# Kernel optimization log

Measured on AMD Instinct MI355X. Metric: run time of the kernel, lower is better.

The kernel has to match this reference:

```python
import jax, jax.numpy as jnp
import numpy as np

K = 5        # kernel_size
G = 1        # group_size
S = 2        # scale_factor
PAD = K // 2


def setup_inputs() -> dict:
    key = jax.random.key(0)
    k1, k2 = jax.random.split(key)
    N, C, H, W = 2, 256, 128, 128
    sH, sW = H * S, W * S
    features = jax.random.normal(k1, (N, C, H, W), dtype=jnp.float32)
    raw = jax.random.uniform(k2, (N, G * K * K, sH, sW), dtype=jnp.float32)
    # CARAFEPack softmax-normalizes masks over the k*k window per group; emulate that here
    m = raw.reshape(N, G, K * K, sH, sW)
    m = m / jnp.sum(m, axis=2, keepdims=True)
    masks = m.reshape(N, G * K * K, sH, sW)
    return {"features": features, "masks": masks}


def _carafe(features, masks):
    N, C, H, W = features.shape
    sH, sW = H * S, W * S
    Cg = C // G
    # zero-pad spatial dims so every output location has a full k x k neighborhood
    fpad = jnp.pad(features, ((0, 0), (0, 0), (PAD, PAD), (PAD, PAD)))  # [N,C,H+2p,W+2p]
    m = masks.reshape(N, G, K * K, sH, sW)
    out = jnp.zeros((N, G, Cg, sH, sW), dtype=features.dtype)
    # loop over the fixed k*k kernel offsets (25 iters): shift, nearest-upsample, weight, accumulate
    for di in range(K):
        for dj in range(K):
            shifted = fpad[:, :, di:di + H, dj:dj + W]                      # [N,C,H,W]
            up = jnp.repeat(jnp.repeat(shifted, S, axis=2), S, axis=3)      # [N,C,sH,sW] nearest upsample
            w = m[:, :, di * K + dj][:, :, None]                            # [N,G,1,sH,sW]
            out = out + up.reshape(N, G, Cg, sH, sW) * w
    return out.reshape(N, C, sH, sW)


def reference(features, masks):
    return _carafe(features, masks)
```

## Files before the change

### kernel.cpp

```cpp
#include <hip/hip_runtime.h>


namespace {
constexpr int N_ = 2, C_ = 256, H_ = 128, W_ = 128;
constexpr int K_ = 5, S_ = 2, PAD_ = 2;
constexpr int SH_ = H_ * S_, SW_ = W_ * S_;
constexpr int CPB = 16;
constexpr int TPB = 256;
constexpr int RPB = 2;
constexpr int HB_ = H_ / RPB;
constexpr int LW  = W_ + 2 * PAD_;
constexpr int LROWS = RPB + 2 * PAD_;
constexpr int LSZ = LROWS * LW;
constexpr int NSLOT = (LSZ + TPB - 1) / TPB;
typedef float v2f __attribute__((ext_vector_type(2)));
}

__device__ __forceinline__ void block_sync_lds() {
    __builtin_amdgcn_sched_barrier(0);
    asm volatile("s_waitcnt lgkmcnt(0)" ::: "memory");
    __builtin_amdgcn_s_barrier();
    __builtin_amdgcn_sched_barrier(0);
}

__global__ __launch_bounds__(TPB, 2) void carafe_kernel(
    const float* __restrict__ feat,
    const float* __restrict__ masks,
    float* __restrict__ out)
{
    __shared__ float lds[2][LSZ];

    const int bx = blockIdx.x;
    const int n  = bx / HB_;
    const int h0 = (bx % HB_) * RPB;
    const int t  = threadIdx.x;
    const int hl = t >> 7;
    const int w  = t & (W_ - 1);
    const int h  = h0 + hl;
    const int c0 = blockIdx.y * CPB;

    int  goff[NSLOT];
    bool gval[NSLOT];
#pragma unroll
    for (int s = 0; s < NSLOT; ++s) {
        int idx = s * TPB + t;
        int r  = idx / LW, cc = idx % LW;
        int gy = h0 - PAD_ + r, gx = cc - PAD_;
        bool ok = (idx < LSZ) && ((unsigned)gy < (unsigned)H_) && ((unsigned)gx < (unsigned)W_);
        gval[s] = ok;
        goff[s] = ok ? (gy * W_ + gx) : 0;
    }

    float m0[25], m1[25], m2[25], m3[25];
    {
        const float* mb = masks + ((size_t)n * 25) * (SH_ * SW_)
                                + (size_t)(S_ * h) * SW_ + S_ * w;
#pragma unroll
        for (int k = 0; k < 25; ++k) {
            v2f tt = *(const v2f*)(mb + (size_t)k * (SH_ * SW_));
            v2f bb = *(const v2f*)(mb + (size_t)k * (SH_ * SW_) + SW_);
            m0[k] = tt.x; m1[k] = tt.y; m2[k] = bb.x; m3[k] = bb.y;
        }
    }

    const float* fb = feat + ((size_t)n * C_ + c0) * (H_ * W_);
    float*       ob = out + (((size_t)n * C_ + c0) * SH_ + (size_t)(S_ * h)) * SW_ + S_ * w;

    auto issue = [&](int c, float* st) {
        const float* f = fb + (size_t)c * (H_ * W_);
#pragma unroll
        for (int s = 0; s < NSLOT; ++s) st[s] = gval[s] ? f[goff[s]] : 0.f;
    };
    auto land = [&](int b, const float* st) {
#pragma unroll
        for (int s = 0; s < NSLOT; ++s) {
            int idx = s * TPB + t;
            if (idx < LSZ) lds[b][idx] = st[s];
        }
    };
    auto compute_store = [&](const float* __restrict__ L, int c) {
        float a0 = 0.f, a1 = 0.f, a2 = 0.f, a3 = 0.f;
#pragma unroll
        for (int di = 0; di < K_; ++di) {
            const float* Lr = L + (hl + di) * LW + w;
            float f0 = Lr[0], f1 = Lr[1], f2 = Lr[2], f3 = Lr[3], f4 = Lr[4];
            const int kb = di * K_;
            a0 = fmaf(f0, m0[kb + 0], a0);
            a1 = fmaf(f0, m1[kb + 0], a1);
            a2 = fmaf(f0, m2[kb + 0], a2);
            a3 = fmaf(f0, m3[kb + 0], a3);
            a0 = fmaf(f1, m0[kb + 1], a0);
            a1 = fmaf(f1, m1[kb + 1], a1);
            a2 = fmaf(f1, m2[kb + 1], a2);
            a3 = fmaf(f1, m3[kb + 1], a3);
            a0 = fmaf(f2, m0[kb + 2], a0);
            a1 = fmaf(f2, m1[kb + 2], a1);
            a2 = fmaf(f2, m2[kb + 2], a2);
            a3 = fmaf(f2, m3[kb + 2], a3);
            a0 = fmaf(f3, m0[kb + 3], a0);
            a1 = fmaf(f3, m1[kb + 3], a1);
            a2 = fmaf(f3, m2[kb + 3], a2);
            a3 = fmaf(f3, m3[kb + 3], a3);
            a0 = fmaf(f4, m0[kb + 4], a0);
            a1 = fmaf(f4, m1[kb + 4], a1);
            a2 = fmaf(f4, m2[kb + 4], a2);
            a3 = fmaf(f4, m3[kb + 4], a3);
        }
        float* oc = ob + (size_t)c * ((size_t)SH_ * SW_);
        v2f top = {a0, a1}, bot = {a2, a3};
        __builtin_nontemporal_store(top, (v2f*)oc);
        __builtin_nontemporal_store(bot, (v2f*)(oc + SW_));
    };

    float stA[NSLOT], stB[NSLOT];
#pragma unroll
    for (int s = 0; s < NSLOT; ++s) {
        int idx = s * TPB + t;
        if (idx < LSZ) lds[0][idx] = gval[s] ? fb[goff[s]] : 0.f;
    }
    issue(1, stA);

    for (int c2 = 0; c2 < CPB; c2 += 2) {
        block_sync_lds();
        if (c2 + 2 < CPB) issue(c2 + 2, stB);
        compute_store(&lds[0][0], c2);
        land(1, stA);

        block_sync_lds();
        if (c2 + 3 < CPB) issue(c2 + 3, stA);
        compute_store(&lds[1][0], c2 + 1);
        if (c2 + 2 < CPB) land(0, stB);
    }
}

extern "C" void kernel_launch(void* const* d_in, const int* in_sizes, int n_in,
                              void* d_out, int out_size, void* d_ws, size_t ws_size,
                              hipStream_t stream) {
    const float* feat  = (const float*)d_in[0];
    const float* masks = (const float*)d_in[1];
    float* out = (float*)d_out;
    dim3 grid(N_ * HB_, C_ / CPB);
    carafe_kernel<<<grid, dim3(TPB), 0, stream>>>(feat, masks, out);
}
```

Baseline: 56.92 us.

## Double channels per pipeline stage and per block, switch to regular stores

Each pipeline stage now loads and computes two channels per LDS buffer instead of one, which halves the barrier count per channel. The block also covers twice as many channels, so mask registers are amortized over more work and the grid is smaller. Nontemporal output stores are replaced with plain vector stores. In exchange, LDS use and staging registers double and there are fewer blocks to fill the GPU.

```diff
diff --git a/kernel.cpp b/kernel.cpp
--- a/kernel.cpp
+++ b/kernel.cpp
@@ -5,7 +5,7 @@
 constexpr int N_ = 2, C_ = 256, H_ = 128, W_ = 128;
 constexpr int K_ = 5, S_ = 2, PAD_ = 2;
 constexpr int SH_ = H_ * S_, SW_ = W_ * S_;
-constexpr int CPB = 16;
+constexpr int CPB = 32;
 constexpr int TPB = 256;
 constexpr int RPB = 2;
 constexpr int HB_ = H_ / RPB;
@@ -28,7 +28,7 @@
     const float* __restrict__ masks,
     float* __restrict__ out)
 {
-    __shared__ float lds[2][LSZ];
+    __shared__ float lds[2][2 * LSZ];
 
     const int bx = blockIdx.x;
     const int n  = bx / HB_;
@@ -66,16 +66,24 @@
     const float* fb = feat + ((size_t)n * C_ + c0) * (H_ * W_);
     float*       ob = out + (((size_t)n * C_ + c0) * SH_ + (size_t)(S_ * h)) * SW_ + S_ * w;
 
-    auto issue = [&](int c, float* st) {
-        const float* f = fb + (size_t)c * (H_ * W_);
+    auto issue2 = [&](int c, float* st) {
+        const float* f0 = fb + (size_t)c * (H_ * W_);
+        const float* f1 = f0 + (H_ * W_);
 #pragma unroll
-        for (int s = 0; s < NSLOT; ++s) st[s] = gval[s] ? f[goff[s]] : 0.f;
+        for (int s = 0; s < NSLOT; ++s) st[s] = gval[s] ? f0[goff[s]] : 0.f;
+#pragma unroll
+        for (int s = 0; s < NSLOT; ++s) st[NSLOT + s] = gval[s] ? f1[goff[s]] : 0.f;
     };
-    auto land = [&](int b, const float* st) {
+    auto land2 = [&](int b, const float* st) {
 #pragma unroll
         for (int s = 0; s < NSLOT; ++s) {
             int idx = s * TPB + t;
             if (idx < LSZ) lds[b][idx] = st[s];
+        }
+#pragma unroll
+        for (int s = 0; s < NSLOT; ++s) {
+            int idx = s * TPB + t;
+            if (idx < LSZ) lds[b][LSZ + idx] = st[NSLOT + s];
         }
     };
     auto compute_store = [&](const float* __restrict__ L, int c) {
@@ -107,29 +115,33 @@
             a3 = fmaf(f4, m3[kb + 4], a3);
         }
         float* oc = ob + (size_t)c * ((size_t)SH_ * SW_);
-        v2f top = {a0, a1}, bot = {a2, a3};
-        __builtin_nontemporal_store(top, (v2f*)oc);
-        __builtin_nontemporal_store(bot, (v2f*)(oc + SW_));
+        *(v2f*)oc         = v2f{a0, a1};
+        *(v2f*)(oc + SW_) = v2f{a2, a3};
     };
 
-    float stA[NSLOT], stB[NSLOT];
+    float stA[2 * NSLOT], stB[2 * NSLOT];
 #pragma unroll
     for (int s = 0; s < NSLOT; ++s) {
         int idx = s * TPB + t;
-        if (idx < LSZ) lds[0][idx] = gval[s] ? fb[goff[s]] : 0.f;
+        if (idx < LSZ) {
+            lds[0][idx]       = gval[s] ? fb[goff[s]] : 0.f;
+            lds[0][LSZ + idx] = gval[s] ? fb[(size_t)(H_ * W_) + goff[s]] : 0.f;
+        }
     }
-    issue(1, stA);
+    issue2(2, stA);
 
-    for (int c2 = 0; c2 < CPB; c2 += 2) {
+    for (int c4 = 0; c4 < CPB; c4 += 4) {
         block_sync_lds();
-        if (c2 + 2 < CPB) issue(c2 + 2, stB);
-        compute_store(&lds[0][0], c2);
-        land(1, stA);
+        if (c4 + 4 < CPB) issue2(c4 + 4, stB);
+        compute_store(&lds[0][0],   c4);
+        compute_store(&lds[0][LSZ], c4 + 1);
+        land2(1, stA);
 
         block_sync_lds();
-        if (c2 + 3 < CPB) issue(c2 + 3, stA);
-        compute_store(&lds[1][0], c2 + 1);
-        if (c2 + 2 < CPB) land(0, stB);
+        if (c4 + 6 < CPB) issue2(c4 + 6, stA);
+        compute_store(&lds[1][0],   c4 + 2);
+        compute_store(&lds[1][LSZ], c4 + 3);
+        if (c4 + 4 < CPB) land2(0, stB);
     }
 }
 
```

Measured after the change: 58.33 us. 1.02x slower.
